# Performance work log

Measured on AMD Instinct MI355X. Metric: run time of the kernel, lower is better.

The kernel has to match this reference:

```python
import jax, jax.numpy as jnp
import numpy as np

B, S, E, H, C = 16, 2048, 128, 768, 457


def setup_inputs() -> dict:
    key = jax.random.key(0)
    ks = jax.random.split(key, 8)
    hidden_states = jax.random.normal(ks[0], (B, S, H), dtype=jnp.float32)
    field_labels = jax.random.randint(ks[1], (B, S), 0, C, dtype=jnp.int64) if jax.config.jax_enable_x64 else jax.random.randint(ks[1], (B, S), 0, C, dtype=jnp.int32)
    label_masks = jax.random.randint(ks[2], (B, S), 0, 2, dtype=jnp.int32)
    entities_attr = jax.random.randint(ks[3], (B, E), 0, C, dtype=jnp.int32)
    entities_list = (jax.random.uniform(ks[4], (B, S, E)) < 0.05).astype(jnp.int32)
    entities_len = jnp.maximum(entities_list.sum(axis=1), 1).astype(jnp.int32)  # (B, E)
    entities_mask = jax.random.randint(ks[5], (B, E), 0, 2).astype(bool)
    W = jax.random.normal(ks[6], (C, H), dtype=jnp.float32) * 0.02
    b = jax.random.normal(ks[7], (C,), dtype=jnp.float32) * 0.02
    return {"hidden_states": hidden_states, "field_labels": field_labels,
            "label_masks": label_masks, "entities_attr": entities_attr,
            "entities_list": entities_list, "entities_len": entities_len,
            "entities_mask": entities_mask, "W": W, "b": b}


def reference(hidden_states, field_labels, label_masks, entities_attr,
              entities_list, entities_len, entities_mask, W, b):
    # Entity mean-pool: torch does (B,E,S,H) expand*mul->sum; algebraically a bmm.
    dt = hidden_states.dtype
    ent_hidden = jnp.einsum('bsh,bse->beh', hidden_states, entities_list.astype(dt))
    ent_hidden = ent_hidden / entities_len.astype(dt)[..., None]        # (B,E,H)
    mc_logits = jnp.einsum('beh,ch->bec', ent_hidden, W) + b             # (B,E,C)
    # masked CrossEntropyLoss (mean over selected entities)
    logp = jax.nn.log_softmax(mc_logits, axis=-1)
    nll = -jnp.take_along_axis(logp, entities_attr[..., None].astype(jnp.int32), axis=-1)[..., 0]
    m = entities_mask.astype(dt)
    mask_loss = (nll * m).sum() / m.sum()
    return mask_loss
```

## Files before the change

### kernel.cpp

```cpp
#include <hip/hip_runtime.h>
#include <hip/hip_bf16.h>
#include <cstdint>
#include <cstddef>

constexpr int Bn = 16, Sn = 2048, En = 128, Hn = 768, Cn = 457;
constexpr int NP = 512;
using f32x4  = __attribute__((ext_vector_type(4))) float;
using bf16x8 = __attribute__((ext_vector_type(8))) short;

static __device__ inline unsigned short f2bf(float x) {
  __hip_bfloat16 b = __float2bfloat16(x);
  return *reinterpret_cast<unsigned short*>(&b);
}
static __device__ inline float bflo(unsigned int u) {
  unsigned int v = u << 16;
  return *reinterpret_cast<float*>(&v);
}
static __device__ inline float bfhi(unsigned int u) {
  unsigned int v = u & 0xFFFF0000u;
  return *reinterpret_cast<float*>(&v);
}

__global__ __launch_bounds__(256) void pack_k(
    const int* __restrict__ el, unsigned int* __restrict__ pk2)
{
  const int l = threadIdx.x & 63;
  const int gw = blockIdx.x * 4 + (threadIdx.x >> 6);
  #pragma unroll 8
  for (int j = 0; j < 8; ++j) {
    const int tok = gw * 8 + j;
    const int b = tok >> 11, s = tok & 2047;
    const int v0 = el[(size_t)tok * 128 + l];
    const int v1 = el[(size_t)tok * 128 + 64 + l];
    const unsigned long long b0 = __ballot(v0 != 0);
    const unsigned long long b1 = __ballot(v1 != 0);
    if (l == 0) {
      unsigned int* p = pk2 + (size_t)b * 4 * Sn + s;
      p[0]          = (unsigned int)b0;
      p[Sn]         = (unsigned int)(b0 >> 32);
      p[2 * Sn]     = (unsigned int)b1;
      p[3 * Sn]     = (unsigned int)(b1 >> 32);
    }
  }
}

constexpr int PBN = 64, PBK = 32, PLD = 40;
constexpr int SCH = 4, SLEN = Sn / SCH, PNK = SLEN / PBK;
__global__ __launch_bounds__(512, 6) void pool_k(
    const float* __restrict__ hidden,
    const unsigned int* __restrict__ pk2,
    unsigned short* __restrict__ entp)
{
  const int b = blockIdx.x, n0 = blockIdx.y * PBN, sc = blockIdx.z;
  const int s0 = sc * SLEN;
  const int tid = threadIdx.x, l = tid & 63, wv = tid >> 6;
  const int wm = wv >> 2, wn = wv & 3;

  __shared__ unsigned short Bs[2][PBN][PLD];
  __shared__ unsigned int   PK2[4 * SLEN];

  {
    const int w = tid >> 7, off = (tid & 127) * 4;
    const uint4 v = *reinterpret_cast<const uint4*>(
        pk2 + (size_t)b * 4 * Sn + (size_t)w * Sn + s0 + off);
    *reinterpret_cast<uint4*>(&PK2[w * SLEN + off]) = v;
  }

  const float* hb = hidden + ((size_t)b * Sn + s0) * Hn + n0;

  auto loadh = [&](int kk, float (&f)[4]) {
    const int sb = kk * PBK + wv * 4;
    f[0] = hb[(size_t)(sb + 0) * Hn + l];
    f[1] = hb[(size_t)(sb + 1) * Hn + l];
    f[2] = hb[(size_t)(sb + 2) * Hn + l];
    f[3] = hb[(size_t)(sb + 3) * Hn + l];
  };

  auto stage_b = [&](int bsel, const float (&f)[4]) {
    uint2 dh;
    dh.x = (unsigned int)f2bf(f[0]) | ((unsigned int)f2bf(f[1]) << 16);
    dh.y = (unsigned int)f2bf(f[2]) | ((unsigned int)f2bf(f[3]) << 16);
    *reinterpret_cast<uint2*>(&Bs[bsel][l][wv * 4]) = dh;
  };

  f32x4 acc[4] = {};
  const int rl = l & 15, q = l >> 4, kr = q * 8;

  auto mfma_step = [&](int k, int cur) {
    const int sbase = k * PBK + kr;
    const bf16x8 bfr =
        *reinterpret_cast<const bf16x8*>(&Bs[cur][wn * 16 + rl][kr]);
    #pragma unroll
    for (int mp = 0; mp < 2; ++mp) {
      const int w = wm * 2 + mp;
      const uint4 u0 = *reinterpret_cast<const uint4*>(&PK2[w * SLEN + sbase]);
      const uint4 u1 = *reinterpret_cast<const uint4*>(&PK2[w * SLEN + sbase + 4]);
      #pragma unroll
      for (int mh = 0; mh < 2; ++mh) {
        const int bi = mh * 16 + rl;
        bf16x8 afr;
        unsigned int* ap = reinterpret_cast<unsigned int*>(&afr);
        ap[0] = (((u0.x >> bi) & 1u) ? 0x3F80u : 0u) |
                (((u0.y >> bi) & 1u) ? 0x3F800000u : 0u);
        ap[1] = (((u0.z >> bi) & 1u) ? 0x3F80u : 0u) |
                (((u0.w >> bi) & 1u) ? 0x3F800000u : 0u);
        ap[2] = (((u1.x >> bi) & 1u) ? 0x3F80u : 0u) |
                (((u1.y >> bi) & 1u) ? 0x3F800000u : 0u);
        ap[3] = (((u1.z >> bi) & 1u) ? 0x3F80u : 0u) |
                (((u1.w >> bi) & 1u) ? 0x3F800000u : 0u);
        acc[mp * 2 + mh] = __builtin_amdgcn_mfma_f32_16x16x32_bf16(
            afr, bfr, acc[mp * 2 + mh], 0, 0, 0);
      }
    }
  };

  float pf[3][4];
  loadh(0, pf[0]);
  loadh(1, pf[1]);
  __syncthreads();
  stage_b(0, pf[0]);
  __syncthreads();

  #pragma unroll
  for (int k = 0; k < PNK; ++k) {
    if (k + 2 < PNK) loadh(k + 2, pf[(k + 2) % 3]);
    mfma_step(k, k & 1);
    if (k + 1 < PNK) stage_b((k + 1) & 1, pf[(k + 1) % 3]);
    __syncthreads();
  }

  unsigned short* dst = entp + (size_t)sc * Bn * En * Hn;
  const int rg = q * 4;
  const int col = n0 + wn * 16 + rl;
  #pragma unroll
  for (int mi = 0; mi < 4; ++mi) {
    #pragma unroll
    for (int r = 0; r < 4; ++r) {
      const int e = wm * 64 + mi * 16 + rg + r;
      dst[(size_t)(b * En + e) * Hn + col] = f2bf(acc[mi][r]);
    }
  }
}

__global__ __launch_bounds__(384) void finalize_k(
    const unsigned short* __restrict__ entp, const int* __restrict__ elen,
    unsigned short* __restrict__ entbf)
{
  const int be = blockIdx.x, t = threadIdx.x;
  const float inv = 1.0f / (float)elen[be];
  constexpr size_t PSu = (size_t)Bn * En * Hn / 2;
  const unsigned int* src =
      reinterpret_cast<const unsigned int*>(entp) + (size_t)be * (Hn / 2) + t;
  float lo = 0.f, hi = 0.f;
  #pragma unroll
  for (int p = 0; p < SCH; ++p) {
    const unsigned int u = src[p * PSu];
    lo += bflo(u);
    hi += bfhi(u);
  }
  const unsigned int out = (unsigned int)f2bf(lo * inv) |
                           ((unsigned int)f2bf(hi * inv) << 16);
  reinterpret_cast<unsigned int*>(entbf)[(size_t)be * (Hn / 2) + t] = out;
}

__global__ __launch_bounds__(256) void cast_w_k(
    const float* __restrict__ Wm, unsigned short* __restrict__ wbf)
{
  const int c = blockIdx.x;
  const int tid = threadIdx.x;
  unsigned short* dst = wbf + (size_t)c * Hn;
  if (c < Cn) {
    const float* src = Wm + (size_t)c * Hn;
    #pragma unroll
    for (int j = 0; j < 3; ++j) dst[tid + j * 256] = f2bf(src[tid + j * 256]);
  } else {
    #pragma unroll
    for (int j = 0; j < 3; ++j) dst[tid + j * 256] = 0;
  }
}

constexpr int BM = 128, BN = 64, BK = 32, LDP = BK + 24;
__global__ __launch_bounds__(256) void gemm_k(
    const unsigned short* __restrict__ A,
    const unsigned short* __restrict__ Bm,
    float* __restrict__ Cm)
{
  __shared__ unsigned short As[BM][LDP];
  __shared__ unsigned short Bs[BN][LDP];
  const int bm = blockIdx.x, bn = blockIdx.y;
  const int tid = threadIdx.x, lane = tid & 63, wv = tid >> 6;
  const int wm = wv >> 1, wn = wv & 1;

  f32x4 acc[4][2] = {};

  for (int k0 = 0; k0 < Hn; k0 += BK) {
    #pragma unroll
    for (int i = 0; i < 2; ++i) {
      const int idx = tid + i * 256;
      const int r = idx >> 2, kc = (idx & 3) * 8;
      const unsigned short* src = A + (size_t)(bm * BM + r) * Hn + k0 + kc;
      *reinterpret_cast<ulonglong2*>(&As[r][kc]) =
          *reinterpret_cast<const ulonglong2*>(src);
    }
    {
      const int r = tid >> 2, kc = (tid & 3) * 8;
      const unsigned short* src = Bm + (size_t)(bn * BN + r) * Hn + k0 + kc;
      *reinterpret_cast<ulonglong2*>(&Bs[r][kc]) =
          *reinterpret_cast<const ulonglong2*>(src);
    }
    __syncthreads();

    const int kr = (lane >> 4) * 8, rl = lane & 15;
    bf16x8 af[4], bf[2];
    #pragma unroll
    for (int mi = 0; mi < 4; ++mi)
      af[mi] = *reinterpret_cast<const bf16x8*>(&As[wm * 64 + mi * 16 + rl][kr]);
    #pragma unroll
    for (int ni = 0; ni < 2; ++ni)
      bf[ni] = *reinterpret_cast<const bf16x8*>(&Bs[wn * 32 + ni * 16 + rl][kr]);
    #pragma unroll
    for (int mi = 0; mi < 4; ++mi)
      #pragma unroll
      for (int ni = 0; ni < 2; ++ni)
        acc[mi][ni] = __builtin_amdgcn_mfma_f32_16x16x32_bf16(
            af[mi], bf[ni], acc[mi][ni], 0, 0, 0);
    __syncthreads();
  }

  const int cl = lane & 15, rg = (lane >> 4) * 4;
  #pragma unroll
  for (int mi = 0; mi < 4; ++mi)
    #pragma unroll
    for (int ni = 0; ni < 2; ++ni) {
      const int col = bn * BN + wn * 32 + ni * 16 + cl;
      #pragma unroll
      for (int r = 0; r < 4; ++r) {
        const int row = bm * BM + wm * 64 + mi * 16 + rg + r;
        Cm[(size_t)row * NP + col] = acc[mi][ni][r];
      }
    }
}

__global__ __launch_bounds__(256) void ce_k(
    const float* __restrict__ logits,
    const float* __restrict__ bv,
    const int* __restrict__ attr,
    const unsigned char* __restrict__ emask,
    float* __restrict__ nll)
{
  const int wv = threadIdx.x >> 6, lane = threadIdx.x & 63;
  const int be = blockIdx.x * 4 + wv;
  if (!emask[be]) { if (lane == 0) nll[be] = 0.f; return; }
  const float* row = logits + (size_t)be * NP;

  float mx = -3.4e38f;
  for (int i = lane; i < Cn; i += 64) mx = fmaxf(mx, row[i] + bv[i]);
  #pragma unroll
  for (int o = 32; o; o >>= 1) mx = fmaxf(mx, __shfl_xor(mx, o, 64));
  float sm = 0.f;
  for (int i = lane; i < Cn; i += 64) sm += __expf(row[i] + bv[i] - mx);
  #pragma unroll
  for (int o = 32; o; o >>= 1) sm += __shfl_xor(sm, o, 64);
  if (lane == 0) {
    const int tg = attr[be];
    nll[be] = mx + logf(sm) - (row[tg] + bv[tg]);
  }
}

__global__ __launch_bounds__(256) void reduce_k(
    const float* __restrict__ nll,
    const unsigned char* __restrict__ emask,
    float* __restrict__ out)
{
  const int tid = threadIdx.x;
  float s = 0.f, c = 0.f;
  for (int i = tid; i < Bn * En; i += 256) {
    s += nll[i];
    c += (float)emask[i];
  }
  #pragma unroll
  for (int o = 32; o; o >>= 1) {
    s += __shfl_xor(s, o, 64);
    c += __shfl_xor(c, o, 64);
  }
  __shared__ float ws_[4], wc_[4];
  const int wave = tid >> 6, lane = tid & 63;
  if (lane == 0) { ws_[wave] = s; wc_[wave] = c; }
  __syncthreads();
  if (tid == 0) {
    out[0] = (ws_[0] + ws_[1] + ws_[2] + ws_[3]) /
             (wc_[0] + wc_[1] + wc_[2] + wc_[3]);
  }
}

extern "C" void kernel_launch(void* const* d_in, const int* in_sizes, int n_in,
                              void* d_out, int out_size, void* d_ws, size_t ws_size,
                              hipStream_t stream) {
  const float* hidden        = (const float*)d_in[0];
  const int* attr            = (const int*)d_in[3];
  const int* el              = (const int*)d_in[4];
  const int* elen            = (const int*)d_in[5];
  const unsigned char* emask = (const unsigned char*)d_in[6];
  const float* Wm            = (const float*)d_in[7];
  const float* bv            = (const float*)d_in[8];

  unsigned short* entbf = (unsigned short*)d_ws;
  unsigned short* wbf   = entbf + (size_t)Bn * En * Hn;
  float* logits = (float*)(wbf + (size_t)NP * Hn);
  float* nll    = logits + (size_t)Bn * En * NP;
  unsigned int* pk2buf = (unsigned int*)(nll + Bn * En);
  unsigned short* entp =
      (unsigned short*)(pk2buf + (size_t)Bn * 4 * Sn);

  hipLaunchKernelGGL(pack_k, dim3(1024), dim3(256), 0, stream, el, pk2buf);
  hipLaunchKernelGGL(pool_k, dim3(Bn, Hn / PBN, SCH), dim3(512), 0, stream,
                     hidden, pk2buf, entp);
  hipLaunchKernelGGL(finalize_k, dim3(Bn * En), dim3(384), 0, stream,
                     entp, elen, entbf);
  hipLaunchKernelGGL(cast_w_k, dim3(NP), dim3(256), 0, stream, Wm, wbf);
  hipLaunchKernelGGL(gemm_k, dim3(Bn * En / BM, NP / BN), dim3(256), 0, stream,
                     entbf, wbf, logits);
  hipLaunchKernelGGL(ce_k, dim3(Bn * En / 4), dim3(256), 0, stream,
                     logits, bv, attr, emask, nll);
  hipLaunchKernelGGL(reduce_k, dim3(1), dim3(256), 0, stream,
                     nll, emask, (float*)d_out);
}
```

Baseline: 63.49 us.

## Double pool K-tile with lighter barriers and shrink GEMM tiles for occupancy

The pooling kernel now stages 64 tokens per iteration instead of 32, halving the number of barrier-separated steps. It replaces __syncthreads with a custom barrier that waits only on LDS counters, and drops the redundant final barrier. The classifier GEMM tile shrinks from 128x64 to 64x32 so more blocks launch and fill the GPU for the small 2048x512 output. Risks are more registers per thread in pool_k, which runs under a 6-blocks-per-SM launch bound, and less data reuse per GEMM block.

```diff
diff --git a/kernel.cpp b/kernel.cpp
--- a/kernel.cpp
+++ b/kernel.cpp
@@ -20,6 +20,14 @@
   unsigned int v = u & 0xFFFF0000u;
   return *reinterpret_cast<float*>(&v);
 }
+
+#define LGKM_BAR()                                            \
+  do {                                                        \
+    asm volatile("s_waitcnt lgkmcnt(0)" ::: "memory");        \
+    __builtin_amdgcn_sched_barrier(0);                        \
+    __builtin_amdgcn_s_barrier();                             \
+    __builtin_amdgcn_sched_barrier(0);                        \
+  } while (0)
 
 __global__ __launch_bounds__(256) void pack_k(
     const int* __restrict__ el, unsigned int* __restrict__ pk2)
@@ -44,8 +52,8 @@
   }
 }
 
-constexpr int PBN = 64, PBK = 32, PLD = 40;
-constexpr int SCH = 4, SLEN = Sn / SCH, PNK = SLEN / PBK;
+constexpr int PBN = 64, PBK2 = 64, PLD2 = 72;
+constexpr int SCH = 4, SLEN = Sn / SCH, PNK2 = SLEN / PBK2;
 __global__ __launch_bounds__(512, 6) void pool_k(
     const float* __restrict__ hidden,
     const unsigned int* __restrict__ pk2,
@@ -56,7 +64,7 @@
   const int tid = threadIdx.x, l = tid & 63, wv = tid >> 6;
   const int wm = wv >> 2, wn = wv & 3;
 
-  __shared__ unsigned short Bs[2][PBN][PLD];
+  __shared__ unsigned short Bs[2][PBN][PLD2];
   __shared__ unsigned int   PK2[4 * SLEN];
 
   {
@@ -68,65 +76,72 @@
 
   const float* hb = hidden + ((size_t)b * Sn + s0) * Hn + n0;
 
-  auto loadh = [&](int kk, float (&f)[4]) {
-    const int sb = kk * PBK + wv * 4;
-    f[0] = hb[(size_t)(sb + 0) * Hn + l];
-    f[1] = hb[(size_t)(sb + 1) * Hn + l];
-    f[2] = hb[(size_t)(sb + 2) * Hn + l];
-    f[3] = hb[(size_t)(sb + 3) * Hn + l];
+  auto loadh = [&](int kk, float (&f)[8]) {
+    const int sb = kk * PBK2 + wv * 8;
+    #pragma unroll
+    for (int i = 0; i < 8; ++i)
+      f[i] = hb[(size_t)(sb + i) * Hn + l];
   };
 
-  auto stage_b = [&](int bsel, const float (&f)[4]) {
-    uint2 dh;
-    dh.x = (unsigned int)f2bf(f[0]) | ((unsigned int)f2bf(f[1]) << 16);
-    dh.y = (unsigned int)f2bf(f[2]) | ((unsigned int)f2bf(f[3]) << 16);
-    *reinterpret_cast<uint2*>(&Bs[bsel][l][wv * 4]) = dh;
+  auto stage_b = [&](int bsel, const float (&f)[8]) {
+    uint2 d0, d1;
+    d0.x = (unsigned int)f2bf(f[0]) | ((unsigned int)f2bf(f[1]) << 16);
+    d0.y = (unsigned int)f2bf(f[2]) | ((unsigned int)f2bf(f[3]) << 16);
+    d1.x = (unsigned int)f2bf(f[4]) | ((unsigned int)f2bf(f[5]) << 16);
+    d1.y = (unsigned int)f2bf(f[6]) | ((unsigned int)f2bf(f[7]) << 16);
+    *reinterpret_cast<uint2*>(&Bs[bsel][l][wv * 8])     = d0;
+    *reinterpret_cast<uint2*>(&Bs[bsel][l][wv * 8 + 4]) = d1;
   };
 
   f32x4 acc[4] = {};
   const int rl = l & 15, q = l >> 4, kr = q * 8;
 
   auto mfma_step = [&](int k, int cur) {
-    const int sbase = k * PBK + kr;
-    const bf16x8 bfr =
-        *reinterpret_cast<const bf16x8*>(&Bs[cur][wn * 16 + rl][kr]);
-    #pragma unroll
-    for (int mp = 0; mp < 2; ++mp) {
-      const int w = wm * 2 + mp;
-      const uint4 u0 = *reinterpret_cast<const uint4*>(&PK2[w * SLEN + sbase]);
-      const uint4 u1 = *reinterpret_cast<const uint4*>(&PK2[w * SLEN + sbase + 4]);
+    #pragma unroll
+    for (int ks = 0; ks < 2; ++ks) {
+      const int sbase = k * PBK2 + ks * 32 + kr;
+      const bf16x8 bfr = *reinterpret_cast<const bf16x8*>(
+          &Bs[cur][wn * 16 + rl][ks * 32 + kr]);
       #pragma unroll
-      for (int mh = 0; mh < 2; ++mh) {
-        const int bi = mh * 16 + rl;
-        bf16x8 afr;
-        unsigned int* ap = reinterpret_cast<unsigned int*>(&afr);
-        ap[0] = (((u0.x >> bi) & 1u) ? 0x3F80u : 0u) |
-                (((u0.y >> bi) & 1u) ? 0x3F800000u : 0u);
-        ap[1] = (((u0.z >> bi) & 1u) ? 0x3F80u : 0u) |
-                (((u0.w >> bi) & 1u) ? 0x3F800000u : 0u);
-        ap[2] = (((u1.x >> bi) & 1u) ? 0x3F80u : 0u) |
-                (((u1.y >> bi) & 1u) ? 0x3F800000u : 0u);
-        ap[3] = (((u1.z >> bi) & 1u) ? 0x3F80u : 0u) |
-                (((u1.w >> bi) & 1u) ? 0x3F800000u : 0u);
-        acc[mp * 2 + mh] = __builtin_amdgcn_mfma_f32_16x16x32_bf16(
-            afr, bfr, acc[mp * 2 + mh], 0, 0, 0);
+      for (int mp = 0; mp < 2; ++mp) {
+        const int w = wm * 2 + mp;
+        const uint4 u0 = *reinterpret_cast<const uint4*>(&PK2[w * SLEN + sbase]);
+        const uint4 u1 = *reinterpret_cast<const uint4*>(&PK2[w * SLEN + sbase + 4]);
+        #pragma unroll
+        for (int mh = 0; mh < 2; ++mh) {
+          const int bi = mh * 16 + rl;
+          bf16x8 afr;
+          unsigned int* ap = reinterpret_cast<unsigned int*>(&afr);
+          ap[0] = (((u0.x >> bi) & 1u) ? 0x3F80u : 0u) |
+                  (((u0.y >> bi) & 1u) ? 0x3F800000u : 0u);
+          ap[1] = (((u0.z >> bi) & 1u) ? 0x3F80u : 0u) |
+                  (((u0.w >> bi) & 1u) ? 0x3F800000u : 0u);
+          ap[2] = (((u1.x >> bi) & 1u) ? 0x3F80u : 0u) |
+                  (((u1.y >> bi) & 1u) ? 0x3F800000u : 0u);
+          ap[3] = (((u1.z >> bi) & 1u) ? 0x3F80u : 0u) |
+                  (((u1.w >> bi) & 1u) ? 0x3F800000u : 0u);
+          acc[mp * 2 + mh] = __builtin_amdgcn_mfma_f32_16x16x32_bf16(
+              afr, bfr, acc[mp * 2 + mh], 0, 0, 0);
+        }
       }
     }
   };
 
-  float pf[3][4];
+  float pf[3][8];
   loadh(0, pf[0]);
   loadh(1, pf[1]);
-  __syncthreads();
+  LGKM_BAR();
   stage_b(0, pf[0]);
-  __syncthreads();
-
-  #pragma unroll
-  for (int k = 0; k < PNK; ++k) {
-    if (k + 2 < PNK) loadh(k + 2, pf[(k + 2) % 3]);
+  LGKM_BAR();
+
+  #pragma unroll
+  for (int k = 0; k < PNK2; ++k) {
+    if (k + 2 < PNK2) loadh(k + 2, pf[(k + 2) % 3]);
     mfma_step(k, k & 1);
-    if (k + 1 < PNK) stage_b((k + 1) & 1, pf[(k + 1) % 3]);
-    __syncthreads();
+    if (k + 1 < PNK2) {
+      stage_b((k + 1) & 1, pf[(k + 1) % 3]);
+      LGKM_BAR();
+    }
   }
 
   unsigned short* dst = entp + (size_t)sc * Bn * En * Hn;
@@ -179,7 +194,7 @@
   }
 }
 
-constexpr int BM = 128, BN = 64, BK = 32, LDP = BK + 24;
+constexpr int BM = 64, BN = 32, BK = 32, LDP = BK + 24;
 __global__ __launch_bounds__(256) void gemm_k(
     const unsigned short* __restrict__ A,
     const unsigned short* __restrict__ Bm,
@@ -191,18 +206,16 @@
   const int tid = threadIdx.x, lane = tid & 63, wv = tid >> 6;
   const int wm = wv >> 1, wn = wv & 1;
 
-  f32x4 acc[4][2] = {};
+  f32x4 acc[2] = {};
 
   for (int k0 = 0; k0 < Hn; k0 += BK) {
-    #pragma unroll
-    for (int i = 0; i < 2; ++i) {
-      const int idx = tid + i * 256;
-      const int r = idx >> 2, kc = (idx & 3) * 8;
+    {
+      const int r = tid >> 2, kc = (tid & 3) * 8;
       const unsigned short* src = A + (size_t)(bm * BM + r) * Hn + k0 + kc;
       *reinterpret_cast<ulonglong2*>(&As[r][kc]) =
           *reinterpret_cast<const ulonglong2*>(src);
     }
-    {
+    if (tid < 128) {
       const int r = tid >> 2, kc = (tid & 3) * 8;
       const unsigned short* src = Bm + (size_t)(bn * BN + r) * Hn + k0 + kc;
       *reinterpret_cast<ulonglong2*>(&Bs[r][kc]) =
@@ -211,34 +224,26 @@
     __syncthreads();
 
     const int kr = (lane >> 4) * 8, rl = lane & 15;
-    bf16x8 af[4], bf[2];
-    #pragma unroll
-    for (int mi = 0; mi < 4; ++mi)
-      af[mi] = *reinterpret_cast<const bf16x8*>(&As[wm * 64 + mi * 16 + rl][kr]);
-    #pragma unroll
-    for (int ni = 0; ni < 2; ++ni)
-      bf[ni] = *reinterpret_cast<const bf16x8*>(&Bs[wn * 32 + ni * 16 + rl][kr]);
-    #pragma unroll
-    for (int mi = 0; mi < 4; ++mi)
-      #pragma unroll
-      for (int ni = 0; ni < 2; ++ni)
-        acc[mi][ni] = __builtin_amdgcn_mfma_f32_16x16x32_bf16(
-            af[mi], bf[ni], acc[mi][ni], 0, 0, 0);
+    const bf16x8 bf = *reinterpret_cast<const bf16x8*>(&Bs[wn * 16 + rl][kr]);
+    #pragma unroll
+    for (int mi = 0; mi < 2; ++mi) {
+      const bf16x8 af =
+          *reinterpret_cast<const bf16x8*>(&As[wm * 32 + mi * 16 + rl][kr]);
+      acc[mi] = __builtin_amdgcn_mfma_f32_16x16x32_bf16(af, bf, acc[mi], 0, 0, 0);
+    }
     __syncthreads();
   }
 
   const int cl = lane & 15, rg = (lane >> 4) * 4;
-  #pragma unroll
-  for (int mi = 0; mi < 4; ++mi)
-    #pragma unroll
-    for (int ni = 0; ni < 2; ++ni) {
-      const int col = bn * BN + wn * 32 + ni * 16 + cl;
-      #pragma unroll
-      for (int r = 0; r < 4; ++r) {
-        const int row = bm * BM + wm * 64 + mi * 16 + rg + r;
-        Cm[(size_t)row * NP + col] = acc[mi][ni][r];
-      }
-    }
+  const int col = bn * BN + wn * 16 + cl;
+  #pragma unroll
+  for (int mi = 0; mi < 2; ++mi) {
+    #pragma unroll
+    for (int r = 0; r < 4; ++r) {
+      const int row = bm * BM + wm * 32 + mi * 16 + rg + r;
+      Cm[(size_t)row * NP + col] = acc[mi][r];
+    }
+  }
 }
 
 __global__ __launch_bounds__(256) void ce_k(
```

Result: no change. 64.46 us (+1.5%).
